# Optimization experiments

Hardware: AMD Instinct MI355X
Metric: run time of the kernel (lower is better)

Reference implementation:

```python
import jax, jax.numpy as jnp
import numpy as np

N, E, D, H, C, L = 50000, 600000, 128, 128, 40, 2
NEG_SLOPE = 0.1


def setup_inputs() -> dict:
    key = jax.random.key(0)
    ks = jax.random.split(key, 12)

    def lin(k, din, dout):
        return (jax.random.normal(k, (din, dout), jnp.float32) / np.sqrt(din)).astype(jnp.float32)

    x = jax.random.normal(ks[0], (N, D), jnp.float32)
    edge_index = jax.random.randint(ks[1], (2, E), 0, N, dtype=jnp.int32)
    return {
        "x": x,
        "edge_index": edge_index,
        "enc_Wl": lin(ks[2], D, H),
        "enc_Wr": lin(ks[3], D, H),
        "enc_b": jnp.zeros((H,), jnp.float32),
        "lay_Wl": jnp.stack([lin(jax.random.fold_in(ks[4], i), H, H) for i in range(L)]),
        "lay_Wr": jnp.stack([lin(jax.random.fold_in(ks[5], i), H, H) for i in range(L)]),
        "lay_b": jnp.zeros((L, H), jnp.float32),
        "dec_Wl": lin(ks[6], H, C),
        "dec_Wr": lin(ks[7], H, C),
        "dec_b": jnp.zeros((C,), jnp.float32),
    }


def _sage(x, src, dst, inv_cnt, Wl, Wr, b):
    # mean-aggregate neighbor messages: gather x[src], scatter-sum to dst, divide by degree
    agg = jax.ops.segment_sum(x[src], dst, num_segments=N) * inv_cnt  # [N, d_in]
    return agg @ Wl + x @ Wr + b


def reference(x, edge_index, enc_Wl, enc_Wr, enc_b, lay_Wl, lay_Wr, lay_b, dec_Wl, dec_Wr, dec_b):
    src, dst = edge_index[0], edge_index[1]
    # in-degree per target node, clamped to 1 (PyG scatter-mean semantics: isolated nodes get 0)
    deg = jax.ops.segment_sum(jnp.ones((E,), jnp.float32), dst, num_segments=N)
    inv_cnt = (1.0 / jnp.maximum(deg, 1.0))[:, None]  # [N, 1]

    h = jax.nn.leaky_relu(_sage(x, src, dst, inv_cnt, enc_Wl, enc_Wr, enc_b), NEG_SLOPE)
    for i in range(L):
        h = jax.nn.leaky_relu(_sage(h, src, dst, inv_cnt, lay_Wl[i], lay_Wr[i], lay_b[i]), NEG_SLOPE)
    out = _sage(h, src, dst, inv_cnt, dec_Wl, dec_Wr, dec_b)
    return jax.nn.log_softmax(out, axis=1)
```

## Files before the change

kernel.cpp:

```cpp
#include <hip/hip_runtime.h>
#include <hip/hip_bf16.h>

#define NN 50000
#define EE 600000
#define HH 128
#define CC 40
#define NEG 0.1f
#define CAP 40
#define NSLOT 50176
#define NBLK (NSLOT / 16)

typedef __attribute__((ext_vector_type(8))) short bf16x8;
typedef __attribute__((ext_vector_type(4))) float f32x4;
typedef __attribute__((ext_vector_type(4))) unsigned uint4v;

__device__ __forceinline__ unsigned short f2bf(float f) {
    unsigned u = __float_as_uint(f);
    unsigned r = u + 0x7fffu + ((u >> 16) & 1u);
    return (unsigned short)(r >> 16);
}
__device__ __forceinline__ float bfhi(unsigned v) { return __uint_as_float(v & 0xFFFF0000u); }
__device__ __forceinline__ float bflo(unsigned v) { return __uint_as_float(v << 16); }

__global__ void k_build(const int* __restrict__ src, const int* __restrict__ dst,
                        int* __restrict__ counts, unsigned short* __restrict__ csr) {
    int e = blockIdx.x * blockDim.x + threadIdx.x;
    if (e < EE) {
        int d = dst[e];
        if ((unsigned)d < (unsigned)NN) {
            int sl = atomicAdd(&counts[d], 1);
            if (sl < CAP) csr[d * CAP + sl] = (unsigned short)src[e];
        }
    }
}

__global__ void k_hist(const int* __restrict__ counts, int* __restrict__ hist) {
    __shared__ int lh[16];
    if (threadIdx.x < 16) lh[threadIdx.x] = 0;
    __syncthreads();
    int n = blockIdx.x * 256 + threadIdx.x;
    if (n < NN) {
        int c = counts[n]; c = c < CAP ? c : CAP;
        atomicAdd(&lh[(c + 3) >> 2], 1);
    }
    __syncthreads();
    if (threadIdx.x < 11) atomicAdd(&hist[threadIdx.x], lh[threadIdx.x]);
}

__global__ void k_prefix(const int* __restrict__ hist, int* __restrict__ base) {
    if (threadIdx.x == 0) {
        int acc = 0;
        for (int r = 10; r >= 0; --r) {
            base[r] = acc;
            acc += (hist[r] + 15) & ~15;
        }
    }
}

__global__ void k_place(const int* __restrict__ counts, const int* __restrict__ base,
                        int* __restrict__ fill, unsigned* __restrict__ perm) {
    __shared__ int lcnt[16];
    __shared__ int lbase[16];
    int t = threadIdx.x;
    if (t < 16) lcnt[t] = 0;
    __syncthreads();
    int n = blockIdx.x * 256 + t;
    int r = 0, lslot = 0, c = 0;
    if (n < NN) {
        c = counts[n]; c = c < CAP ? c : CAP;
        r = (c + 3) >> 2;
        lslot = atomicAdd(&lcnt[r], 1);
    }
    __syncthreads();
    if (t < 11 && lcnt[t] > 0) lbase[t] = atomicAdd(&fill[t], lcnt[t]);
    __syncthreads();
    if (n < NN) {
        int slot = base[r] + lbase[r] + lslot;
        if (slot >= 0 && slot < NSLOT) perm[slot] = (unsigned)n | ((unsigned)c << 16);
    }
}

struct PrepArgs {
    const float* wsrc[8];
    unsigned short* wdst[8];
    int* counts;
    const float* x;
    unsigned* xb;
    unsigned* perm;
    int* aux;
};

template <int DOUT, int DOUTP>
__device__ __forceinline__ void swz_one(const float* __restrict__ W,
                                        unsigned short* __restrict__ dstf, int idx) {
    int k = idx / DOUTP, n = idx % DOUTP;
    unsigned short val = (n < DOUT) ? f2bf(W[k * DOUT + n]) : (unsigned short)0;
    int kt = k >> 5, kin = k & 31, nt = n >> 4, nin = n & 15;
    int lane = ((kin >> 3) << 4) | nin;
    int j = kin & 7;
    int NT = DOUTP >> 4;
    dstf[(((kt * NT + nt) * 64) + lane) * 8 + j] = val;
}

#define XCB ((NN * HH / 4 + 255) / 256)
#define PFB ((NSLOT + 255) / 256)

__global__ void k_prep(PrepArgs a) {
    int b = blockIdx.x;
    if (b < 384) {
        int tid = b * 256 + threadIdx.x;
        if (tid < NN) a.counts[tid] = 0;
        int which = b >> 6;
        int idx = (b & 63) * 256 + threadIdx.x;
        swz_one<HH, HH>(a.wsrc[which], a.wdst[which], idx);
    } else if (b < 432) {
        int bb = b - 384;
        int which = 6 + bb / 24;
        int idx = (bb % 24) * 256 + threadIdx.x;
        swz_one<CC, 48>(a.wsrc[which], a.wdst[which], idx);
    } else if (b < 432 + XCB) {
        int t = (b - 432) * 256 + threadIdx.x;
        if (t < NN * HH / 4) {
            float4 v = ((const float4*)a.x)[t];
            uint2 o;
            o.x = ((unsigned)f2bf(v.y) << 16) | f2bf(v.x);
            o.y = ((unsigned)f2bf(v.w) << 16) | f2bf(v.z);
            ((uint2*)a.xb)[t] = o;
        }
    } else {
        int i = (b - (432 + XCB)) * 256 + threadIdx.x;
        if (i < NSLOT) a.perm[i] = 0xFFFFFFFFu;
        if (i < 64) a.aux[i] = 0;
    }
}

template <int R>
__device__ __forceinline__ void gather_batch(const unsigned long long* cw,
                                             const uint4v* __restrict__ hw4,
                                             int s, int sh16, int gg, int cnt, int base_r,
                                             float (&acc)[8]) {
    uint4v vb[R];
#pragma unroll
    for (int r = 0; r < R; ++r) {
        unsigned long long w = cw[base_r + r];
        unsigned half = (s & 2) ? (unsigned)(w >> 32) : (unsigned)w;
        unsigned idx = (half >> sh16) & 0xffffu;
        idx = idx < (unsigned)NN ? idx : 0u;
        vb[r] = hw4[(size_t)idx * 16 + gg];
    }
#pragma unroll
    for (int r = 0; r < R; ++r) {
        if ((base_r + r) * 4 + s < cnt) {
            acc[0] += bflo(vb[r].x); acc[1] += bfhi(vb[r].x);
            acc[2] += bflo(vb[r].y); acc[3] += bfhi(vb[r].y);
            acc[4] += bflo(vb[r].z); acc[5] += bfhi(vb[r].z);
            acc[6] += bflo(vb[r].w); acc[7] += bfhi(vb[r].w);
        }
    }
}

template <int MODE>
__global__ __launch_bounds__(1024, 8) void k_layer(
    const unsigned short* __restrict__ hin,
    const unsigned* __restrict__ perm,
    const unsigned short* __restrict__ csr,
    const unsigned short* __restrict__ B1f, const unsigned short* __restrict__ B2f,
    const float* __restrict__ bias, unsigned short* __restrict__ out,
    const unsigned short* __restrict__ Tf, unsigned short* __restrict__ tOut) {
    __shared__ unsigned lds[16][72];
    __shared__ unsigned selfLds[16][68];
    __shared__ int nodeTab[16];
    int wid = threadIdx.x >> 6;
    int lane = threadIdx.x & 63;
    int m0 = blockIdx.x * 16;
    int gg = lane & 15;
    int s = lane >> 4;
    int sh16 = (s & 1) * 16;
    const uint4v* hw4 = (const uint4v*)hin;

    int slot = __builtin_amdgcn_readfirstlane(m0 + wid);
    unsigned pe = perm[slot];
    int node = (int)(pe & 0xffffu);
    int cnt = (int)((pe >> 16) & 0xffffu);
    int valid = node < NN;
    if (lane == 0) nodeTab[wid] = valid ? node : (1 << 30);
    int rounds = valid ? (cnt + 3) >> 2 : 0;
    rounds = rounds < 10 ? rounds : 10;
    float sc = 1.0f / (float)((valid && cnt > 0) ? cnt : 1);

    if (lane < 16) {
        uint4v sv = hw4[(size_t)(valid ? node : 0) * 16 + lane];
        *(uint4v*)&selfLds[wid][lane * 4] = sv;
    }

    const unsigned long long* cr8 =
        (const unsigned long long*)(csr + (size_t)(valid ? node : 0) * CAP);
    unsigned long long cw[10];
#pragma unroll
    for (int r = 0; r < 10; ++r) cw[r] = cr8[r];

    float acc[8];
#pragma unroll
    for (int d = 0; d < 8; ++d) acc[d] = 0.f;

    switch (rounds) {
        case 0: break;
        case 1: gather_batch<1>(cw, hw4, s, sh16, gg, cnt, 0, acc); break;
        case 2: gather_batch<2>(cw, hw4, s, sh16, gg, cnt, 0, acc); break;
        case 3: gather_batch<3>(cw, hw4, s, sh16, gg, cnt, 0, acc); break;
        case 4: gather_batch<4>(cw, hw4, s, sh16, gg, cnt, 0, acc); break;
        case 5: gather_batch<5>(cw, hw4, s, sh16, gg, cnt, 0, acc); break;
        case 6: gather_batch<3>(cw, hw4, s, sh16, gg, cnt, 0, acc);
                gather_batch<3>(cw, hw4, s, sh16, gg, cnt, 3, acc); break;
        case 7: gather_batch<4>(cw, hw4, s, sh16, gg, cnt, 0, acc);
                gather_batch<3>(cw, hw4, s, sh16, gg, cnt, 4, acc); break;
        case 8: gather_batch<4>(cw, hw4, s, sh16, gg, cnt, 0, acc);
                gather_batch<4>(cw, hw4, s, sh16, gg, cnt, 4, acc); break;
        case 9: gather_batch<5>(cw, hw4, s, sh16, gg, cnt, 0, acc);
                gather_batch<4>(cw, hw4, s, sh16, gg, cnt, 5, acc); break;
        default: gather_batch<5>(cw, hw4, s, sh16, gg, cnt, 0, acc);
                 gather_batch<5>(cw, hw4, s, sh16, gg, cnt, 5, acc); break;
    }

#pragma unroll
    for (int d = 0; d < 8; ++d) {
        float t = acc[d];
        t += __shfl_xor(t, 16, 64);
        t += __shfl_xor(t, 32, 64);
        acc[d] = t * sc;
    }
    if (lane < 16) {
        unsigned w4[4];
        w4[0] = ((unsigned)f2bf(acc[1]) << 16) | f2bf(acc[0]);
        w4[1] = ((unsigned)f2bf(acc[3]) << 16) | f2bf(acc[2]);
        w4[2] = ((unsigned)f2bf(acc[5]) << 16) | f2bf(acc[4]);
        w4[3] = ((unsigned)f2bf(acc[7]) << 16) | f2bf(acc[6]);
        *(uint4v*)&lds[wid][gg * 4] = *(uint4v*)w4;
    }
    __syncthreads();

    int nin = lane & 15;
    int kq = lane >> 4;
    unsigned short hv[4];

    if (wid < 8) {
        const unsigned* arow = &lds[nin][0];
        const unsigned short* srow = (const unsigned short*)&selfLds[nin][0];
        f32x4 acc1 = (f32x4){0.f, 0.f, 0.f, 0.f};

#pragma unroll
        for (int kt = 0; kt < 4; ++kt) {
            bf16x8 a1 = *(const bf16x8*)(arow + kt * 16 + kq * 4);
            bf16x8 a2 = *(const bf16x8*)(srow + kt * 32 + kq * 8);
            bf16x8 b1 = *(const bf16x8*)(B1f + (((kt * 8 + wid) * 64) + lane) * 8);
            acc1 = __builtin_amdgcn_mfma_f32_16x16x32_bf16(a1, b1, acc1, 0, 0, 0);
            bf16x8 b2 = *(const bf16x8*)(B2f + (((kt * 8 + wid) * 64) + lane) * 8);
            acc1 = __builtin_amdgcn_mfma_f32_16x16x32_bf16(a2, b2, acc1, 0, 0, 0);
        }

        int col = wid * 16 + nin;
        float bv = bias[col];
#pragma unroll
        for (int r = 0; r < 4; ++r) {
            float v = acc1[r] + bv;
            v = fmaxf(v, NEG * v);
            hv[r] = f2bf(v);
        }
    }

    __syncthreads();
    unsigned short* lsh = (unsigned short*)&lds[0][0];
    if (wid < 8) {
        int col = wid * 16 + nin;
#pragma unroll
        for (int r = 0; r < 4; ++r) lsh[(kq * 4 + r) * 144 + col] = hv[r];
    }
    __syncthreads();
    {
        int nm = nodeTab[wid];
        if (nm < NN && lane < 16)
            *(uint4v*)&out[(size_t)nm * HH + lane * 8] = *(uint4v*)&lsh[wid * 144 + lane * 8];
    }

    if (MODE == 1) {
        if (wid < 3) {
            f32x4 at = (f32x4){0.f, 0.f, 0.f, 0.f};
#pragma unroll
            for (int kt = 0; kt < 4; ++kt) {
                bf16x8 a = *(const bf16x8*)&lsh[nin * 144 + kt * 32 + kq * 8];
                bf16x8 b = *(const bf16x8*)(Tf + (((kt * 3 + wid) * 64) + lane) * 8);
                at = __builtin_amdgcn_mfma_f32_16x16x32_bf16(a, b, at, 0, 0, 0);
            }
#pragma unroll
            for (int r = 0; r < 4; ++r) {
                int nm = nodeTab[kq * 4 + r];
                if (nm < NN) tOut[(size_t)nm * 48 + wid * 16 + nin] = f2bf(at[r]);
            }
        }
    }
}

template <int R>
__device__ __forceinline__ void gatherd_batch(const unsigned long long* cw,
                                              const uint4v* __restrict__ t4,
                                              int s, int sh16, int g6, int cnt,
                                              float (&acc)[8]) {
    uint4v vb[R];
#pragma unroll
    for (int r = 0; r < R; ++r) {
        unsigned long long w = (s & 4) ? cw[2 * r + 1] : cw[2 * r];
        unsigned half = (s & 2) ? (unsigned)(w >> 32) : (unsigned)w;
        unsigned idx = (half >> sh16) & 0xffffu;
        idx = idx < (unsigned)NN ? idx : 0u;
        vb[r] = t4[(size_t)idx * 6 + g6];
    }
#pragma unroll
    for (int r = 0; r < R; ++r) {
        if (r * 8 + s < cnt) {
            acc[0] += bflo(vb[r].x); acc[1] += bfhi(vb[r].x);
            acc[2] += bflo(vb[r].y); acc[3] += bfhi(vb[r].y);
            acc[4] += bflo(vb[r].z); acc[5] += bfhi(vb[r].z);
            acc[6] += bflo(vb[r].w); acc[7] += bfhi(vb[r].w);
        }
    }
}

__global__ __launch_bounds__(1024, 8) void k_dec(
    const unsigned short* __restrict__ tbuf,
    const unsigned short* __restrict__ h1,
    const unsigned* __restrict__ perm,
    const unsigned short* __restrict__ csr,
    const unsigned short* __restrict__ B2f, const float* __restrict__ bias,
    float* __restrict__ out) {
    __shared__ float aggT[16][52];
    __shared__ int nodeTab[16];
    int wid = threadIdx.x >> 6;
    int lane = threadIdx.x & 63;
    int m0 = blockIdx.x * 16;
    int g = lane & 7;
    int g6 = g < 6 ? g : g - 6;
    int s = lane >> 3;
    int sh16 = (s & 1) * 16;
    const uint4v* t4 = (const uint4v*)tbuf;

    int slot = __builtin_amdgcn_readfirstlane(m0 + wid);
    unsigned pe = perm[slot];
    int node = (int)(pe & 0xffffu);
    int cnt = (int)((pe >> 16) & 0xffffu);
    int valid = node < NN;
    if (lane == 0) nodeTab[wid] = valid ? node : (1 << 30);
    int rounds = valid ? (cnt + 7) >> 3 : 0;
    rounds = rounds < 5 ? rounds : 5;
    float sc = 1.0f / (float)((valid && cnt > 0) ? cnt : 1);

    const unsigned long long* cr8 =
        (const unsigned long long*)(csr + (size_t)(valid ? node : 0) * CAP);
    unsigned long long cw[10];
#pragma unroll
    for (int r = 0; r < 10; ++r) cw[r] = cr8[r];

    float acc[8];
#pragma unroll
    for (int d = 0; d < 8; ++d) acc[d] = 0.f;

    switch (rounds) {
        case 0: break;
        case 1: gatherd_batch<1>(cw, t4, s, sh16, g6, cnt, acc); break;
        case 2: gatherd_batch<2>(cw, t4, s, sh16, g6, cnt, acc); break;
        case 3: gatherd_batch<3>(cw, t4, s, sh16, g6, cnt, acc); break;
        case 4: gatherd_batch<4>(cw, t4, s, sh16, g6, cnt, acc); break;
        default: gatherd_batch<5>(cw, t4, s, sh16, g6, cnt, acc); break;
    }

#pragma unroll
    for (int d = 0; d < 8; ++d) {
        float t = acc[d];
        t += __shfl_xor(t, 8, 64);
        t += __shfl_xor(t, 16, 64);
        t += __shfl_xor(t, 32, 64);
        acc[d] = t * sc;
    }
    if (s == 0 && g < 6) {
        float4 p0, p1;
        p0.x = acc[0]; p0.y = acc[1]; p0.z = acc[2]; p0.w = acc[3];
        p1.x = acc[4]; p1.y = acc[5]; p1.z = acc[6]; p1.w = acc[7];
        *(float4*)&aggT[wid][8 * g] = p0;
        *(float4*)&aggT[wid][8 * g + 4] = p1;
    }
    __syncthreads();
    if (wid != 0) return;

    int nin = lane & 15, kq = lane >> 4;
    int node2 = nodeTab[nin];
    int na = node2 < NN ? node2 : 0;
    f32x4 acc2[3];
#pragma unroll
    for (int j = 0; j < 3; ++j) acc2[j] = (f32x4){0.f, 0.f, 0.f, 0.f};
#pragma unroll
    for (int kt = 0; kt < 4; ++kt) {
        bf16x8 a2 = *(const bf16x8*)(h1 + (size_t)na * HH + kt * 32 + kq * 8);
#pragma unroll
        for (int j = 0; j < 3; ++j) {
            bf16x8 b2 = *(const bf16x8*)(B2f + (((kt * 3 + j) * 64) + lane) * 8);
            acc2[j] = __builtin_amdgcn_mfma_f32_16x16x32_bf16(a2, b2, acc2[j], 0, 0, 0);
        }
    }
    float bv[3];
#pragma unroll
    for (int t = 0; t < 3; ++t) {
        int col = t * 16 + nin;
        bv[t] = (col < CC) ? bias[col] : 0.f;
    }
#pragma unroll
    for (int r = 0; r < 4; ++r) {
        int ml = kq * 4 + r;
        int nm = nodeTab[ml];
        float v[3];
        float mx = -1e30f;
#pragma unroll
        for (int t = 0; t < 3; ++t) {
            int col = t * 16 + nin;
            v[t] = acc2[t][r] + aggT[ml][col] + bv[t];
            if (col < CC) mx = fmaxf(mx, v[t]);
        }
        for (int off = 1; off < 16; off <<= 1) mx = fmaxf(mx, __shfl_xor(mx, off, 64));
        float sm = 0.f;
#pragma unroll
        for (int t = 0; t < 3; ++t) {
            int col = t * 16 + nin;
            if (col < CC) sm += expf(v[t] - mx);
        }
        for (int off = 1; off < 16; off <<= 1) sm += __shfl_xor(sm, off, 64);
        float lse = mx + logf(sm);
#pragma unroll
        for (int t = 0; t < 3; ++t) {
            int col = t * 16 + nin;
            if (col < CC && nm < NN) out[(size_t)nm * CC + col] = v[t] - lse;
        }
    }
}

extern "C" void kernel_launch(void* const* d_in, const int* in_sizes, int n_in,
                              void* d_out, int out_size, void* d_ws, size_t ws_size,
                              hipStream_t stream) {
    const float* x      = (const float*)d_in[0];
    const int*   ei     = (const int*)d_in[1];
    const float* enc_Wl = (const float*)d_in[2];
    const float* enc_Wr = (const float*)d_in[3];
    const float* enc_b  = (const float*)d_in[4];
    const float* lay_Wl = (const float*)d_in[5];
    const float* lay_Wr = (const float*)d_in[6];
    const float* lay_b  = (const float*)d_in[7];
    const float* dec_Wl = (const float*)d_in[8];
    const float* dec_Wr = (const float*)d_in[9];
    const float* dec_b  = (const float*)d_in[10];
    float* out = (float*)d_out;

    const int* src = ei;
    const int* dst = ei + EE;

    char* p = (char*)d_ws;
    auto carve = [&](size_t bytes) {
        char* r = p;
        p += (bytes + 255) & ~(size_t)255;
        return r;
    };
    int*            counts = (int*)carve(NN * 4);
    unsigned short* csr    = (unsigned short*)carve((size_t)NN * CAP * 2);
    unsigned short* h1     = (unsigned short*)carve((size_t)NN * HH * 2);
    unsigned short* h2     = (unsigned short*)carve((size_t)NN * HH * 2);
    unsigned short* tbuf   = (unsigned short*)carve((size_t)NN * 48 * 2 + 256);
    unsigned*       perm   = (unsigned*)carve((size_t)NSLOT * 4);
    int*            aux    = (int*)carve(64 * 4);
    unsigned short* wf[8];
    for (int i = 0; i < 6; ++i) wf[i] = (unsigned short*)carve(HH * HH * 2);
    wf[6] = (unsigned short*)carve(HH * 48 * 2);
    wf[7] = (unsigned short*)carve(HH * 48 * 2);

    {
        PrepArgs a;
        a.wsrc[0] = enc_Wl; a.wsrc[1] = enc_Wr;
        a.wsrc[2] = lay_Wl; a.wsrc[3] = lay_Wr;
        a.wsrc[4] = lay_Wl + HH * HH; a.wsrc[5] = lay_Wr + HH * HH;
        a.wsrc[6] = dec_Wl; a.wsrc[7] = dec_Wr;
        for (int i = 0; i < 8; ++i) a.wdst[i] = wf[i];
        a.counts = counts;
        a.x = x;
        a.xb = (unsigned*)h2;
        a.perm = perm;
        a.aux = aux;
        k_prep<<<432 + XCB + PFB, 256, 0, stream>>>(a);
    }

    k_build<<<(EE + 255) / 256, 256, 0, stream>>>(src, dst, counts, csr);
    k_hist<<<(NN + 255) / 256, 256, 0, stream>>>(counts, aux);
    k_prefix<<<1, 64, 0, stream>>>(aux, aux + 32);
    k_place<<<(NN + 255) / 256, 256, 0, stream>>>(counts, aux + 32, aux + 16, perm);

    k_layer<0><<<NBLK, 1024, 0, stream>>>(h2, perm, csr, wf[0], wf[1], enc_b,      h1, nullptr, nullptr);
    k_layer<0><<<NBLK, 1024, 0, stream>>>(h1, perm, csr, wf[2], wf[3], lay_b,      h2, nullptr, nullptr);
    k_layer<1><<<NBLK, 1024, 0, stream>>>(h2, perm, csr, wf[4], wf[5], lay_b + HH, h1, wf[6], tbuf);

    k_dec<<<NBLK, 1024, 0, stream>>>(tbuf, h1, perm, csr, wf[7], dec_b, out);
}
```

Measured before the change: 308.4 us.

## Pad decoder table to 64 columns, coalesce stores, drop perm in decoder

```diff
diff --git a/kernel.cpp b/kernel.cpp
--- a/kernel.cpp
+++ b/kernel.cpp
@@ -9,6 +9,7 @@
 #define CAP 40
 #define NSLOT 50176
 #define NBLK (NSLOT / 16)
+#define DBLK (NN / 16)
 
 typedef __attribute__((ext_vector_type(8))) short bf16x8;
 typedef __attribute__((ext_vector_type(4))) float f32x4;
@@ -283,6 +284,7 @@
     }
 
     if (MODE == 1) {
+        unsigned short* tsh = (unsigned short*)&selfLds[0][0];
         if (wid < 3) {
             f32x4 at = (f32x4){0.f, 0.f, 0.f, 0.f};
 #pragma unroll
@@ -292,10 +294,16 @@
                 at = __builtin_amdgcn_mfma_f32_16x16x32_bf16(a, b, at, 0, 0, 0);
             }
 #pragma unroll
-            for (int r = 0; r < 4; ++r) {
-                int nm = nodeTab[kq * 4 + r];
-                if (nm < NN) tOut[(size_t)nm * 48 + wid * 16 + nin] = f2bf(at[r]);
-            }
+            for (int r = 0; r < 4; ++r) tsh[(kq * 4 + r) * 64 + wid * 16 + nin] = f2bf(at[r]);
+        } else if (wid == 3) {
+#pragma unroll
+            for (int r = 0; r < 4; ++r) tsh[(kq * 4 + r) * 64 + 48 + nin] = 0;
+        }
+        __syncthreads();
+        {
+            int nm = nodeTab[wid];
+            if (nm < NN && lane < 8)
+                *(uint4v*)&tOut[(size_t)nm * 64 + lane * 8] = *(uint4v*)&tsh[wid * 64 + lane * 8];
         }
     }
 }
@@ -303,7 +311,7 @@
 template <int R>
 __device__ __forceinline__ void gatherd_batch(const unsigned long long* cw,
                                               const uint4v* __restrict__ t4,
-                                              int s, int sh16, int g6, int cnt,
+                                              int s, int sh16, int g, int cnt,
                                               float (&acc)[8]) {
     uint4v vb[R];
 #pragma unroll
@@ -312,7 +320,7 @@
         unsigned half = (s & 2) ? (unsigned)(w >> 32) : (unsigned)w;
         unsigned idx = (half >> sh16) & 0xffffu;
         idx = idx < (unsigned)NN ? idx : 0u;
-        vb[r] = t4[(size_t)idx * 6 + g6];
+        vb[r] = t4[(size_t)idx * 8 + g];
     }
 #pragma unroll
     for (int r = 0; r < R; ++r) {
@@ -328,33 +336,35 @@
 __global__ __launch_bounds__(1024, 8) void k_dec(
     const unsigned short* __restrict__ tbuf,
     const unsigned short* __restrict__ h1,
-    const unsigned* __restrict__ perm,
+    const int* __restrict__ counts,
     const unsigned short* __restrict__ csr,
     const unsigned short* __restrict__ B2f, const float* __restrict__ bias,
     float* __restrict__ out) {
-    __shared__ float aggT[16][52];
-    __shared__ int nodeTab[16];
+    __shared__ float aggT[16][68];
+    __shared__ unsigned selfLds[16][68];
+    __shared__ float ldsOut[16][40];
     int wid = threadIdx.x >> 6;
     int lane = threadIdx.x & 63;
     int m0 = blockIdx.x * 16;
     int g = lane & 7;
-    int g6 = g < 6 ? g : g - 6;
     int s = lane >> 3;
     int sh16 = (s & 1) * 16;
     const uint4v* t4 = (const uint4v*)tbuf;
-
-    int slot = __builtin_amdgcn_readfirstlane(m0 + wid);
-    unsigned pe = perm[slot];
-    int node = (int)(pe & 0xffffu);
-    int cnt = (int)((pe >> 16) & 0xffffu);
-    int valid = node < NN;
-    if (lane == 0) nodeTab[wid] = valid ? node : (1 << 30);
-    int rounds = valid ? (cnt + 7) >> 3 : 0;
-    rounds = rounds < 5 ? rounds : 5;
-    float sc = 1.0f / (float)((valid && cnt > 0) ? cnt : 1);
-
-    const unsigned long long* cr8 =
-        (const unsigned long long*)(csr + (size_t)(valid ? node : 0) * CAP);
+    const uint4v* h4 = (const uint4v*)h1;
+
+    int node = m0 + wid;
+    int cnt = counts[node];
+    cnt = __builtin_amdgcn_readfirstlane(cnt);
+    cnt = cnt < CAP ? cnt : CAP;
+    int rounds = (cnt + 7) >> 3;
+    float sc = 1.0f / (float)(cnt > 0 ? cnt : 1);
+
+    if (lane < 16) {
+        uint4v sv = h4[(size_t)node * 16 + lane];
+        *(uint4v*)&selfLds[wid][lane * 4] = sv;
+    }
+
+    const unsigned long long* cr8 = (const unsigned long long*)(csr + (size_t)node * CAP);
     unsigned long long cw[10];
 #pragma unroll
     for (int r = 0; r < 10; ++r) cw[r] = cr8[r];
@@ -365,11 +375,11 @@
 
     switch (rounds) {
         case 0: break;
-        case 1: gatherd_batch<1>(cw, t4, s, sh16, g6, cnt, acc); break;
-        case 2: gatherd_batch<2>(cw, t4, s, sh16, g6, cnt, acc); break;
-        case 3: gatherd_batch<3>(cw, t4, s, sh16, g6, cnt, acc); break;
-        case 4: gatherd_batch<4>(cw, t4, s, sh16, g6, cnt, acc); break;
-        default: gatherd_batch<5>(cw, t4, s, sh16, g6, cnt, acc); break;
+        case 1: gatherd_batch<1>(cw, t4, s, sh16, g, cnt, acc); break;
+        case 2: gatherd_batch<2>(cw, t4, s, sh16, g, cnt, acc); break;
+        case 3: gatherd_batch<3>(cw, t4, s, sh16, g, cnt, acc); break;
+        case 4: gatherd_batch<4>(cw, t4, s, sh16, g, cnt, acc); break;
+        default: gatherd_batch<5>(cw, t4, s, sh16, g, cnt, acc); break;
     }
 
 #pragma unroll
@@ -380,64 +390,63 @@
         t += __shfl_xor(t, 32, 64);
         acc[d] = t * sc;
     }
-    if (s == 0 && g < 6) {
-        float4 p0, p1;
-        p0.x = acc[0]; p0.y = acc[1]; p0.z = acc[2]; p0.w = acc[3];
-        p1.x = acc[4]; p1.y = acc[5]; p1.z = acc[6]; p1.w = acc[7];
-        *(float4*)&aggT[wid][8 * g] = p0;
-        *(float4*)&aggT[wid][8 * g + 4] = p1;
-    }
-    __syncthreads();
-    if (wid != 0) return;
-
-    int nin = lane & 15, kq = lane >> 4;
-    int node2 = nodeTab[nin];
-    int na = node2 < NN ? node2 : 0;
-    f32x4 acc2[3];
-#pragma unroll
-    for (int j = 0; j < 3; ++j) acc2[j] = (f32x4){0.f, 0.f, 0.f, 0.f};
-#pragma unroll
-    for (int kt = 0; kt < 4; ++kt) {
-        bf16x8 a2 = *(const bf16x8*)(h1 + (size_t)na * HH + kt * 32 + kq * 8);
-#pragma unroll
-        for (int j = 0; j < 3; ++j) {
-            bf16x8 b2 = *(const bf16x8*)(B2f + (((kt * 3 + j) * 64) + lane) * 8);
-            acc2[j] = __builtin_amdgcn_mfma_f32_16x16x32_bf16(a2, b2, acc2[j], 0, 0, 0);
-        }
-    }
-    float bv[3];
-#pragma unroll
-    for (int t = 0; t < 3; ++t) {
-        int col = t * 16 + nin;
-        bv[t] = (col < CC) ? bias[col] : 0.f;
-    }
-#pragma unroll
-    for (int r = 0; r < 4; ++r) {
-        int ml = kq * 4 + r;
-        int nm = nodeTab[ml];
-        float v[3];
-        float mx = -1e30f;
+    if (s == 0) {
+        *(float4*)&aggT[wid][g * 8]     = *(float4*)&acc[0];
+        *(float4*)&aggT[wid][g * 8 + 4] = *(float4*)&acc[4];
+    }
+    __syncthreads();
+
+    if (wid == 0) {
+        int nin = lane & 15, kq = lane >> 4;
+        const unsigned short* srow = (const unsigned short*)&selfLds[nin][0];
+        f32x4 acc2[3];
+#pragma unroll
+        for (int j = 0; j < 3; ++j) acc2[j] = (f32x4){0.f, 0.f, 0.f, 0.f};
+#pragma unroll
+        for (int kt = 0; kt < 4; ++kt) {
+            bf16x8 a2 = *(const bf16x8*)(srow + kt * 32 + kq * 8);
+#pragma unroll
+            for (int j = 0; j < 3; ++j) {
+                bf16x8 b2 = *(const bf16x8*)(B2f + (((kt * 3 + j) * 64) + lane) * 8);
+                acc2[j] = __builtin_amdgcn_mfma_f32_16x16x32_bf16(a2, b2, acc2[j], 0, 0, 0);
+            }
+        }
+        float bv[3];
 #pragma unroll
         for (int t = 0; t < 3; ++t) {
             int col = t * 16 + nin;
-            v[t] = acc2[t][r] + aggT[ml][col] + bv[t];
-            if (col < CC) mx = fmaxf(mx, v[t]);
-        }
-        for (int off = 1; off < 16; off <<= 1) mx = fmaxf(mx, __shfl_xor(mx, off, 64));
-        float sm = 0.f;
-#pragma unroll
-        for (int t = 0; t < 3; ++t) {
-            int col = t * 16 + nin;
-            if (col < CC) sm += expf(v[t] - mx);
-        }
-        for (int off = 1; off < 16; off <<= 1) sm += __shfl_xor(sm, off, 64);
-        float lse = mx + logf(sm);
-#pragma unroll
-        for (int t = 0; t < 3; ++t) {
-            int col = t * 16 + nin;
-            if (col < CC && nm < NN) out[(size_t)nm * CC + col] = v[t] - lse;
-        }
-    }
+            bv[t] = (col < CC) ? bias[col] : 0.f;
+        }
+#pragma unroll
+        for (int r = 0; r < 4; ++r) {
+            int ml = kq * 4 + r;
+            float v[3];
+            float mx = -1e30f;
+#pragma unroll
+            for (int t = 0; t < 3; ++t) {
+                int col = t * 16 + nin;
+                v[t] = acc2[t][r] + aggT[ml][col] + bv[t];
+                if (col < CC) mx = fmaxf(mx, v[t]);
+            }
+            for (int off = 1; off < 16; off <<= 1) mx = fmaxf(mx, __shfl_xor(mx, off, 64));
+            float sm = 0.f;
+#pragma unroll
+            for (int t = 0; t < 3; ++t) {
+                int col = t * 16 + nin;
+                if (col < CC) sm += expf(v[t] - mx);
+            }
+            for (int off = 1; off < 16; off <<= 1) sm += __shfl_xor(sm, off, 64);
+            float lse = mx + logf(sm);
+#pragma unroll
+            for (int t = 0; t < 3; ++t) {
+                int col = t * 16 + nin;
+                if (col < CC) ldsOut[ml][col] = v[t] - lse;
+            }
+        }
+    }
+    __syncthreads();
+    int tid = threadIdx.x;
+    if (tid < 16 * CC) out[(size_t)m0 * CC + tid] = ((const float*)ldsOut)[tid];
 }
 
 extern "C" void kernel_launch(void* const* d_in, const int* in_sizes, int n_in,
@@ -469,7 +478,7 @@
     unsigned short* csr    = (unsigned short*)carve((size_t)NN * CAP * 2);
     unsigned short* h1     = (unsigned short*)carve((size_t)NN * HH * 2);
     unsigned short* h2     = (unsigned short*)carve((size_t)NN * HH * 2);
-    unsigned short* tbuf   = (unsigned short*)carve((size_t)NN * 48 * 2 + 256);
+    unsigned short* tbuf   = (unsigned short*)carve((size_t)NN * 64 * 2 + 256);
     unsigned*       perm   = (unsigned*)carve((size_t)NSLOT * 4);
     int*            aux    = (int*)carve(64 * 4);
     unsigned short* wf[8];
@@ -501,5 +510,5 @@
     k_layer<0><<<NBLK, 1024, 0, stream>>>(h1, perm, csr, wf[2], wf[3], lay_b,      h2, nullptr, nullptr);
     k_layer<1><<<NBLK, 1024, 0, stream>>>(h2, perm, csr, wf[4], wf[5], lay_b + HH, h1, wf[6], tbuf);
 
-    k_dec<<<NBLK, 1024, 0, stream>>>(tbuf, h1, perm, csr, wf[7], dec_b, out);
-}
+    k_dec<<<DBLK, 1024, 0, stream>>>(tbuf, h1, counts, csr, wf[7], dec_b, out);
+}
```

New measurement: 314.2 us. Within noise of the previous version (+1.9%).
